# Kernel tuning notes

Measured on AMD Instinct MI355X. Metric: run time of the kernel, lower is better.

## Reference

```python
import jax, jax.numpy as jnp
import numpy as np

MULT = 0.001      # DEFAULT_MULTIPLIER
N_ITERS = 9       # self.N
N_K = 4           # self.l
BINARY = ('mul', 'add')  # original binary_ops_list order


def _valid_pairs(nc, r, lc):
    # replicate flag logic over (i, j) candidate pairs
    nri = N_ITERS - r
    out = []
    for i in range(nc - 1):
        for j in range(i + 1, nc):
            if nri == lc - 1:
                flag = i >= 3
            elif nri == lc:
                flag = j >= 3
            else:
                flag = nri > lc
            if flag:
                out.append((i, j))
    return out


def _act(name, res):
    if name == 'sigmoid':
        return MULT * jax.nn.sigmoid(res)
    if name == 'tanh':
        return MULT * jnp.tanh(res)
    if name == 'minus':
        return 1.0 - res
    return res  # identity


def run_cell(x, h_prev, L, R, b, w, plan=None):
    """Faithful RRNNforGRUCell tree-structure search.
    record mode (plan=None): data-dependent decisions taken concretely (eager).
    replay mode (plan given): purely differentiable jnp replay of recorded plan.
    """
    record = plan is None
    if record:
        plan = []
    xv = x.reshape(-1)
    hv = h_prev.reshape(-1)
    H = xv.shape[0]
    zero = jnp.zeros((H,), dtype=xv.dtype)
    G = []            # max_vector per iteration
    second = []       # second-ranked vector per iteration
    comp_src = []     # G-indices backing current components_list
    for r in range(N_ITERS):
        cand = [xv, hv, zero] + [G[g] for g in comp_src]
        nc = len(cand)
        C = jnp.stack(cand)                       # (nc, H)
        CL = jnp.einsum('ch,khd->ckd', C, L)      # (nc, 4, H) all s_i @ L_k
        CR = jnp.einsum('ch,khd->ckd', C, R)      # (nc, 4, H) all s_j @ R_k
        V = []
        if record:
            entries = []
            for (i, j) in _valid_pairs(nc, r, len(comp_src)):
                for k in range(N_K):
                    for bf in BINARY:
                        if bf == 'mul':
                            res = CL[i, k] * CR[j, k] + b[k]
                        else:
                            res = CL[i, k] + CR[j, k] + b[k]
                        if float(jnp.max(jnp.abs(res))) >= 1.0:
                            acts = ('sigmoid', 'tanh')
                        else:
                            acts = ('sigmoid', 'tanh', 'minus', 'identity')
                        for a in acts:
                            V.append(_act(a, res))
                            entries.append((i, j, k, bf, a))
        else:
            entries = plan[r]['entries']
            cache = {}
            for (i, j, k, bf, a) in entries:
                key = (i, j, k, bf)
                if key not in cache:
                    if bf == 'mul':
                        cache[key] = CL[i, k] * CR[j, k] + b[k]
                    else:
                        cache[key] = CL[i, k] + CR[j, k] + b[k]
                V.append(_act(a, cache[key]))
        Vs = jnp.stack(V)          # (nV, H)
        scores = Vs @ w            # (nV,) scoring Linear(H,1,bias=False)
        if record:
            s = np.asarray(scores)
            max_idx = int(np.argmax(s))
            # position of the element ranked second-smallest (original code)
            second_idx = int(np.where(np.argsort(s) == 1)[0][0])
            plan.append({'entries': entries, 'max_idx': max_idx, 'second_idx': second_idx})
        else:
            max_idx = plan[r]['max_idx']
            second_idx = plan[r]['second_idx']
        probs = jax.nn.softmax(scores)
        # NOTE: replicates original bug: loop uses stale `i` == nc-2, so every
        # v is weighted by probabilities[nc-2].
        max_vec = probs[nc - 2] * Vs.sum(axis=0)
        second.append(V[second_idx])
        G.append(max_vec)
        i, j = entries[max_idx][0], entries[max_idx][1]
        if i > 2 and j > 2:
            comp_src[i - 3] = r
            del comp_src[j - 3]
        elif i <= 2 and j > 2:
            comp_src[j - 3] = r
        else:
            comp_src.append(r)
    Gs = jnp.stack(G)                       # (9, H)
    out = (Gs[-1], Gs, Gs @ w, jnp.stack(second) @ w)
    return (out, plan) if record else out


def setup_inputs() -> dict:
    key = jax.random.key(0)
    ks = jax.random.split(key, 6)
    H = 2048
    return {
        'x': jax.random.normal(ks[0], (1, H), jnp.float32),
        'h_prev': jax.random.normal(ks[1], (1, H), jnp.float32),
        'L': MULT * jax.random.normal(ks[2], (N_K, H, H), jnp.float32),
        'R': MULT * jax.random.normal(ks[3], (N_K, H, H), jnp.float32),
        'b': MULT * jax.random.normal(ks[4], (N_K, H), jnp.float32),
        'w': jax.random.normal(ks[5], (H,), jnp.float32),
    }


def reference(x, h_prev, L, R, b, w):
    # returns (h_next, G_stack [9,H], scores of G [9], second_scores [9])
    out, _ = run_cell(x, h_prev, L, R, b, w)
    return out
```

## Files before the change

kernel.cpp:

```cpp
#include <hip/hip_runtime.h>
#include <math.h>

#define HDIM 2048
#define NK 4
#define NIT 9
#define NSID 11
#define MAXPAIRS 36
#define MAXBASES (MAXPAIRS*8)

#define CACHE_SZ (NSID*2*NK*HDIM)
#define OFF_CACHE 0
#define OFF_AMAX   (OFF_CACHE + CACHE_SZ)
#define OFF_DOTR_D (OFF_AMAX + MAXBASES)
#define OFF_DOTS_D (OFF_DOTR_D + 2*MAXBASES)
#define OFF_DOTT_D (OFF_DOTS_D + 2*MAXBASES)
#define PLAN_SZ 152
#define OFF_PLAN0 (OFF_DOTT_D + 2*MAXBASES)
#define OFF_PLAN1 (OFF_PLAN0 + PLAN_SZ)
#define OFF_SEL   (OFF_PLAN1 + PLAN_SZ)
#define OFF_STATE (OFF_SEL + 16)
#define OFF_SUMW_D (OFF_STATE + 16)
#define OFF_GT8   (OFF_SUMW_D + 16)
#define OFF_PART  (OFF_GT8 + 8*HDIM)

#define SEL_PSEL 0
#define SEL_C4   1

__device__ __forceinline__ float wredmax(float v){
#pragma unroll
  for(int o=32;o;o>>=1) v = fmaxf(v,__shfl_down(v,o,64));
  return v;
}
__device__ __forceinline__ float wredsum(float v){
#pragma unroll
  for(int o=32;o;o>>=1) v += __shfl_down(v,o,64);
  return v;
}
__device__ __forceinline__ double wredsumd(double v){
#pragma unroll
  for(int o=32;o;o>>=1) v += __shfl_down(v,o,64);
  return v;
}

__device__ void build_plan(int r, int lc, const int* cs, int* plan){
  int nc = 3 + lc;
  int nri = NIT - r;
  int np = 0;
  for(int i=0;i<nc-1;i++){
    for(int j=i+1;j<nc;j++){
      bool flag;
      if (nri == lc-1)      flag = (i>=3);
      else if (nri == lc)   flag = (j>=3);
      else                  flag = (nri > lc);
      if(flag){
        plan[8+np]            = i;
        plan[8+MAXPAIRS+np]   = j;
        plan[8+2*MAXPAIRS+np] = (i<3)? i : 3+cs[i-3];
        plan[8+3*MAXPAIRS+np] = (j<3)? j : 3+cs[j-3];
        np++;
      }
    }
  }
  plan[0]=nc; plan[1]=np; plan[2]=np*8;
}

__global__ __launch_bounds__(256) void kinit(const float* __restrict__ w,
                                             float* __restrict__ ws,
                                             float* __restrict__ out){
  for(int i=blockIdx.x*256+threadIdx.x; i<8*HDIM; i+=gridDim.x*256)
    ws[OFF_CACHE + 16*HDIM + i] = 0.f;
  if (blockIdx.x == 0){
    double s = 0.0;
    for(int d=threadIdx.x; d<HDIM; d+=256) s += (double)w[d];
    s = wredsumd(s);
    __shared__ double red[4];
    int wv = threadIdx.x>>6, ln = threadIdx.x&63;
    if(!ln) red[wv]=s;
    __syncthreads();
    if(threadIdx.x==0){
      *(double*)(ws + OFF_SUMW_D) = red[0]+red[1]+red[2]+red[3];
      int* st = (int*)(ws + OFF_STATE);
      for(int q=0;q<=8;q++) st[q]=0;
      build_plan(0, 0, st+1, (int*)(ws + OFF_PLAN0));
    }
    if (threadIdx.x < 18) out[10*HDIM + threadIdx.x] = 0.f;
  }
}

__global__ __launch_bounds__(256) void kvecmat(const float* __restrict__ v,
                                               const float* __restrict__ L,
                                               const float* __restrict__ R,
                                               float* __restrict__ ws){
  __shared__ float vs[64];
  int combo = blockIdx.x >> 6;
  int m = combo >> 2, k = combo & 3;
  int rem = blockIdx.x & 63;
  int hc = rem >> 1, dc = rem & 1;
  int h0 = hc*64;
  int d0 = dc*1024 + threadIdx.x*4;
  if (threadIdx.x < 64) vs[threadIdx.x] = v[h0 + threadIdx.x];
  __syncthreads();
  const float* M = (m==0?L:R) + (size_t)k*HDIM*HDIM;
  float ax=0.f, ay=0.f, az=0.f, aw=0.f;
#pragma unroll 8
  for(int h=0; h<64; h++){
    const float4 f = *reinterpret_cast<const float4*>(M + (size_t)(h0+h)*HDIM + d0);
    float vv = vs[h];
    ax = fmaf(vv, f.x, ax); ay = fmaf(vv, f.y, ay);
    az = fmaf(vv, f.z, az); aw = fmaf(vv, f.w, aw);
  }
  float4 o; o.x=ax; o.y=ay; o.z=az; o.w=aw;
  *reinterpret_cast<float4*>(ws + OFF_PART + ((size_t)combo*32 + hc)*HDIM + d0) = o;
}

__global__ __launch_bounds__(256) void kreduce(float* __restrict__ ws, int sid){
  int combo = blockIdx.x >> 3;
  int dc = blockIdx.x & 7;
  int d = dc*256 + threadIdx.x;
  const float* p = ws + OFF_PART + (size_t)combo*32*HDIM + d;
  float s = 0.f;
#pragma unroll
  for(int hc=0; hc<32; hc++) s += p[(size_t)hc*HDIM];
  int m = combo>>2, k = combo&3;
  ws[OFF_CACHE + ((size_t)(sid*2+m)*NK + k)*HDIM + d] = s;
}

__global__ __launch_bounds__(256) void kbasestats(const float* __restrict__ bvec,
                                                  const float* __restrict__ w,
                                                  float* __restrict__ ws, int par){
  const int* plan = (const int*)(ws + (par ? OFF_PLAN1 : OFF_PLAN0));
  int nb = plan[2];
  int t = blockIdx.x;
  if (t >= nb) return;
  int p = t>>3, k=(t>>1)&3, bf=t&1;
  int si = plan[8+2*MAXPAIRS+p], sj = plan[8+3*MAXPAIRS+p];
  const float* CL = ws + OFF_CACHE + ((size_t)(si*2+0)*NK + k)*HDIM;
  const float* CR = ws + OFF_CACHE + ((size_t)(sj*2+1)*NK + k)*HDIM;
  const float* bk = bvec + (size_t)k*HDIM;
  float am=0.f; double dr=0.0, ds=0.0, dt=0.0;
  for(int d=threadIdx.x; d<HDIM; d+=256){
    float a = CL[d], c = CR[d];
    float res = (bf==0) ? __fadd_rn(__fmul_rn(a,c), bk[d])
                        : __fadd_rn(__fadd_rn(a,c), bk[d]);
    float wd = w[d];
    am = fmaxf(am, fabsf(res));
    float sg = 1.0f/(1.0f+expf(-res));
    float th = tanhf(res);
    dr += (double)res*(double)wd;
    ds += (double)sg *(double)wd;
    dt += (double)th *(double)wd;
  }
  am = wredmax(am); dr = wredsumd(dr); ds = wredsumd(ds); dt = wredsumd(dt);
  __shared__ double redd[4][3];
  __shared__ float  redm[4];
  int wv = threadIdx.x>>6, ln = threadIdx.x&63;
  if(!ln){ redm[wv]=am; redd[wv][0]=dr; redd[wv][1]=ds; redd[wv][2]=dt; }
  __syncthreads();
  if(!threadIdx.x){
    float A=redm[0]; double Dr=redd[0][0], Ds=redd[0][1], Dt=redd[0][2];
    for(int q=1;q<4;q++){ A=fmaxf(A,redm[q]); Dr+=redd[q][0]; Ds+=redd[q][1]; Dt+=redd[q][2]; }
    ws[OFF_AMAX+t]=A;
    ((double*)(ws+OFF_DOTR_D))[t]=Dr;
    ((double*)(ws+OFF_DOTS_D))[t]=Ds;
    ((double*)(ws+OFF_DOTT_D))[t]=Dt;
  }
}

__global__ __launch_bounds__(256) void kselect(float* __restrict__ ws,
                                               float* __restrict__ out, int r){
  __shared__ double s4[MAXBASES][4];
  __shared__ int    sna[MAXBASES];
  __shared__ double tval[256];
  __shared__ int    tidx[256];
  __shared__ double tz[256];
  __shared__ int    tcnt[256];
  __shared__ double sh_smax;
  int par = r & 1;
  int* plan = (int*)(ws + (par ? OFF_PLAN1 : OFF_PLAN0));
  int nc = plan[0];
  int nb = plan[2];
  double sumw = *(const double*)(ws + OFF_SUMW_D);
  const double* DR = (const double*)(ws+OFF_DOTR_D);
  const double* DS = (const double*)(ws+OFF_DOTS_D);
  const double* DT = (const double*)(ws+OFF_DOTT_D);
  int tid = threadIdx.x;
  for(int t=tid; t<nb; t+=256){
    float A  = ws[OFF_AMAX+t];
    double Dr = DR[t], Ds = DS[t], Dt = DT[t];
    sna[t] = (A < 1.0f) ? 4 : 2;
    s4[t][0] = 0.001*Ds;
    s4[t][1] = 0.001*Dt;
    s4[t][2] = sumw - Dr;
    s4[t][3] = Dr;
  }
  __syncthreads();
  double best = -1e300; int bidx = 1<<30;
  for(int q=tid; q<nb*4; q+=256){
    int t=q>>2, a=q&3;
    if (a < sna[t]){
      double v = s4[t][a];
      if (v > best || (v==best && q < bidx)){ best=v; bidx=q; }
    }
  }
  tval[tid]=best; tidx[tid]=bidx;
  __syncthreads();
  if (tid==0){
    double bb=tval[0]; int bi=tidx[0];
    for(int u=1;u<256;u++)
      if (tval[u] > bb || (tval[u]==bb && tidx[u] < bi)){ bb=tval[u]; bi=tidx[u]; }
    sh_smax = bb;
    tidx[0] = bi;
  }
  __syncthreads();
  double smax = sh_smax;
  double s1 = s4[0][1];
  double z = 0.0; int cnt = 0;
  for(int q=tid; q<nb*4; q+=256){
    int t=q>>2, a=q&3;
    if (a < sna[t]){
      double v = s4[t][a];
      z += exp(v - smax);
      cnt += (v < s1) ? 1 : 0;
    }
  }
  tz[tid]=z; tcnt[tid]=cnt;
  __syncthreads();
  if (tid==0){
    int bi = tidx[0];
    double Z=0.0; int rank=0;
    for(int u=0;u<256;u++){ Z += tz[u]; rank += tcnt[u]; }
    int need = nc-2, e=0; double s_sel=0.0;
    for(int t=0;t<nb;t++){
      int n = sna[t];
      if (need < e+n){ s_sel = s4[t][need-e]; break; }
      e += n;
    }
    double psel = exp(s_sel - smax) / Z;
    int e2=0; double ssec=0.0;
    for(int t=0;t<nb;t++){
      int n = sna[t];
      if (rank < e2+n){ ssec = s4[t][rank-e2]; break; }
      e2 += n;
    }
    out[10*HDIM + 9 + r] = (float)ssec;
    int c4=0;
    for(int t=0;t<nb;t++) c4 += (sna[t]==4) ? 1 : 0;
    int mt = bi>>2;
    int mp = mt>>3;
    int ci = plan[8+mp], cj = plan[8+MAXPAIRS+mp];
    float* sel = ws + OFF_SEL;
    int*  seli = (int*)sel;
    sel[SEL_PSEL] = (float)psel;
    seli[SEL_C4]  = c4;
    int* st = (int*)(ws + OFF_STATE);
    int lc = st[0];
    int* cs = st+1;
    if (ci>2 && cj>2){
      cs[ci-3] = r;
      for(int q2=cj-3; q2<lc-1; q2++) cs[q2]=cs[q2+1];
      lc--;
    } else if (ci<=2 && cj>2){
      cs[cj-3] = r;
    } else {
      cs[lc] = r; lc++;
    }
    st[0]=lc;
    if (r+1 < NIT)
      build_plan(r+1, lc, cs, (int*)(ws + ((par^1) ? OFF_PLAN1 : OFF_PLAN0)));
  }
}

__global__ __launch_bounds__(256) void kaccum(const float* __restrict__ bvec,
                                              float* __restrict__ ws, int r){
  int par = r & 1;
  const int* plan = (const int*)(ws + (par ? OFF_PLAN1 : OFF_PLAN0));
  int nb = plan[2];
  int bc = blockIdx.x >> 3;
  int db = blockIdx.x & 7;
  int d = db*256 + threadIdx.x;
  float acc = 0.f;
  for(int t=bc; t<nb; t+=8){
    int p=t>>3, k=(t>>1)&3, bf=t&1;
    int si = plan[8+2*MAXPAIRS+p], sj = plan[8+3*MAXPAIRS+p];
    float a = ws[OFF_CACHE + ((size_t)(si*2+0)*NK+k)*HDIM + d];
    float c = ws[OFF_CACHE + ((size_t)(sj*2+1)*NK+k)*HDIM + d];
    float res = (bf==0) ? (a*c + bvec[(size_t)k*HDIM+d]) : (a + c + bvec[(size_t)k*HDIM+d]);
    float ex  = __expf(-res);
    float sig = 1.0f/(1.0f+ex);
    float ex2 = ex*ex;
    float th  = (1.0f-ex2)/(1.0f+ex2);
    acc += sig + th;
  }
  ws[OFF_GT8 + (size_t)bc*HDIM + d] = acc;
}

__global__ __launch_bounds__(256) void kfinal(const float* __restrict__ w,
                                              float* __restrict__ ws,
                                              float* __restrict__ out, int r){
  int d = blockIdx.x*256 + threadIdx.x;
  const float* sel = ws + OFF_SEL;
  const int*  seli = (const int*)sel;
  float psel = sel[SEL_PSEL];
  int  c4   = seli[SEL_C4];
  float s = 0.f;
#pragma unroll
  for(int bc=0; bc<8; bc++) s += ws[OFF_GT8 + (size_t)bc*HDIM + d];
  float g = psel * (0.001f*s + (float)c4);
  out[HDIM + (size_t)r*HDIM + d] = g;
  if (r == NIT-1) out[d] = g;
  float gw = wredsum(g*w[d]);
  __shared__ float red[4];
  int wv = threadIdx.x>>6, ln = threadIdx.x&63;
  if(!ln) red[wv]=gw;
  __syncthreads();
  if(!threadIdx.x)
    atomicAdd(&out[10*HDIM + r], red[0]+red[1]+red[2]+red[3]);
}

extern "C" void kernel_launch(void* const* d_in, const int* in_sizes, int n_in,
                              void* d_out, int out_size, void* d_ws, size_t ws_size,
                              hipStream_t stream){
  const float* x = (const float*)d_in[0];
  const float* h = (const float*)d_in[1];
  const float* L = (const float*)d_in[2];
  const float* R = (const float*)d_in[3];
  const float* b = (const float*)d_in[4];
  const float* w = (const float*)d_in[5];
  float* out = (float*)d_out;
  float* ws  = (float*)d_ws;

  kinit<<<32,256,0,stream>>>(w, ws, out);
  kvecmat<<<512,256,0,stream>>>(x, L, R, ws);
  kreduce<<<64,256,0,stream>>>(ws, 0);
  kvecmat<<<512,256,0,stream>>>(h, L, R, ws);
  kreduce<<<64,256,0,stream>>>(ws, 1);
  for(int r=0;r<NIT;r++){
    if (r > 0){
      kvecmat<<<512,256,0,stream>>>(out + HDIM + (size_t)(r-1)*HDIM, L, R, ws);
      kreduce<<<64,256,0,stream>>>(ws, 3+(r-1));
    }
    kbasestats<<<MAXBASES,256,0,stream>>>(b, w, ws, r&1);
    kselect<<<1,256,0,stream>>>(ws, out, r);
    kaccum<<<64,256,0,stream>>>(b, ws, r);
    kfinal<<<8,256,0,stream>>>(w, ws, out, r);
  }
}
```

Before: 601.7 us.

## Fuse per-iteration kernels and batch initial vector-matrix products

Folds the init work into the first vecmat launch, runs the x and h vector-matrix products in one launch, and merges basestats with accum and select with final. This cuts the launch count per iteration from six to four and removes the atomic and workspace round-trip for the selection scalars. The vecmat tiling is also changed from float4 to float2 loads over smaller column chunks, doubling block count. kselfin now does the final pass with a single block, which serializes 2048 elements of work onto one block.

```diff
diff --git a/kernel.cpp b/kernel.cpp
--- a/kernel.cpp
+++ b/kernel.cpp
@@ -17,14 +17,10 @@
 #define PLAN_SZ 152
 #define OFF_PLAN0 (OFF_DOTT_D + 2*MAXBASES)
 #define OFF_PLAN1 (OFF_PLAN0 + PLAN_SZ)
-#define OFF_SEL   (OFF_PLAN1 + PLAN_SZ)
-#define OFF_STATE (OFF_SEL + 16)
+#define OFF_STATE (OFF_PLAN1 + PLAN_SZ)
 #define OFF_SUMW_D (OFF_STATE + 16)
 #define OFF_GT8   (OFF_SUMW_D + 16)
 #define OFF_PART  (OFF_GT8 + 8*HDIM)
-
-#define SEL_PSEL 0
-#define SEL_C4   1
 
 __device__ __forceinline__ float wredmax(float v){
 #pragma unroll
@@ -64,109 +60,136 @@
   plan[0]=nc; plan[1]=np; plan[2]=np*8;
 }
 
-__global__ __launch_bounds__(256) void kinit(const float* __restrict__ w,
-                                             float* __restrict__ ws,
-                                             float* __restrict__ out){
-  for(int i=blockIdx.x*256+threadIdx.x; i<8*HDIM; i+=gridDim.x*256)
-    ws[OFF_CACHE + 16*HDIM + i] = 0.f;
-  if (blockIdx.x == 0){
-    double s = 0.0;
-    for(int d=threadIdx.x; d<HDIM; d+=256) s += (double)w[d];
-    s = wredsumd(s);
-    __shared__ double red[4];
-    int wv = threadIdx.x>>6, ln = threadIdx.x&63;
-    if(!ln) red[wv]=s;
-    __syncthreads();
-    if(threadIdx.x==0){
-      *(double*)(ws + OFF_SUMW_D) = red[0]+red[1]+red[2]+red[3];
-      int* st = (int*)(ws + OFF_STATE);
-      for(int q=0;q<=8;q++) st[q]=0;
-      build_plan(0, 0, st+1, (int*)(ws + OFF_PLAN0));
-    }
-    if (threadIdx.x < 18) out[10*HDIM + threadIdx.x] = 0.f;
-  }
-}
-
-__global__ __launch_bounds__(256) void kvecmat(const float* __restrict__ v,
+__global__ __launch_bounds__(256) void kvecmat(const float* __restrict__ va,
+                                               const float* __restrict__ vb,
+                                               const float* __restrict__ w,
                                                const float* __restrict__ L,
                                                const float* __restrict__ R,
-                                               float* __restrict__ ws){
+                                               float* __restrict__ ws,
+                                               int nvec){
+  int bid = blockIdx.x;
+  int tid = threadIdx.x;
+  if (bid >= (nvec<<10)){
+    int ib = bid - (nvec<<10);
+    for(int i = ib*256+tid; i < 8*HDIM; i += 32*256)
+      ws[OFF_CACHE + 16*HDIM + i] = 0.f;
+    if (ib == 0){
+      double s = 0.0;
+      for(int d=tid; d<HDIM; d+=256) s += (double)w[d];
+      s = wredsumd(s);
+      __shared__ double red[4];
+      int wv = tid>>6, ln = tid&63;
+      if(!ln) red[wv]=s;
+      __syncthreads();
+      if(tid==0){
+        *(double*)(ws + OFF_SUMW_D) = red[0]+red[1]+red[2]+red[3];
+        int* st = (int*)(ws + OFF_STATE);
+        for(int q=0;q<=8;q++) st[q]=0;
+        build_plan(0, 0, st+1, (int*)(ws + OFF_PLAN0));
+      }
+    }
+    return;
+  }
+  int vec = bid >> 10;
+  int b   = bid & 1023;
+  int combo = b >> 7;
+  int hc    = (b >> 2) & 31;
+  int dc    = b & 3;
+  const float* v = vec ? vb : va;
   __shared__ float vs[64];
-  int combo = blockIdx.x >> 6;
-  int m = combo >> 2, k = combo & 3;
-  int rem = blockIdx.x & 63;
-  int hc = rem >> 1, dc = rem & 1;
-  int h0 = hc*64;
-  int d0 = dc*1024 + threadIdx.x*4;
-  if (threadIdx.x < 64) vs[threadIdx.x] = v[h0 + threadIdx.x];
-  __syncthreads();
-  const float* M = (m==0?L:R) + (size_t)k*HDIM*HDIM;
-  float ax=0.f, ay=0.f, az=0.f, aw=0.f;
+  if (tid < 64) vs[tid] = v[hc*64 + tid];
+  __syncthreads();
+  int m = combo>>2, k = combo&3;
+  const float* M = (m==0?L:R) + (size_t)k*HDIM*HDIM + (size_t)hc*64*HDIM + dc*512 + tid*2;
+  float ax=0.f, ay=0.f;
 #pragma unroll 8
   for(int h=0; h<64; h++){
-    const float4 f = *reinterpret_cast<const float4*>(M + (size_t)(h0+h)*HDIM + d0);
+    const float2 f = *reinterpret_cast<const float2*>(M + (size_t)h*HDIM);
     float vv = vs[h];
     ax = fmaf(vv, f.x, ax); ay = fmaf(vv, f.y, ay);
-    az = fmaf(vv, f.z, az); aw = fmaf(vv, f.w, aw);
-  }
-  float4 o; o.x=ax; o.y=ay; o.z=az; o.w=aw;
-  *reinterpret_cast<float4*>(ws + OFF_PART + ((size_t)combo*32 + hc)*HDIM + d0) = o;
-}
-
-__global__ __launch_bounds__(256) void kreduce(float* __restrict__ ws, int sid){
-  int combo = blockIdx.x >> 3;
-  int dc = blockIdx.x & 7;
-  int d = dc*256 + threadIdx.x;
-  const float* p = ws + OFF_PART + (size_t)combo*32*HDIM + d;
+  }
+  float2 o; o.x=ax; o.y=ay;
+  *reinterpret_cast<float2*>(ws + OFF_PART + ((size_t)(vec*8+combo)*32 + hc)*HDIM + dc*512 + tid*2) = o;
+}
+
+__global__ __launch_bounds__(256) void kreduce(float* __restrict__ ws, int sid0){
+  int b = blockIdx.x;
+  int vec = b>>6, rem = b&63;
+  int combo = rem>>3, dc8 = rem&7;
+  int d = dc8*256 + threadIdx.x;
+  const float* p = ws + OFF_PART + (size_t)(vec*8+combo)*32*HDIM + d;
   float s = 0.f;
 #pragma unroll
   for(int hc=0; hc<32; hc++) s += p[(size_t)hc*HDIM];
   int m = combo>>2, k = combo&3;
+  int sid = sid0 + vec;
   ws[OFF_CACHE + ((size_t)(sid*2+m)*NK + k)*HDIM + d] = s;
 }
 
-__global__ __launch_bounds__(256) void kbasestats(const float* __restrict__ bvec,
+__global__ __launch_bounds__(256) void kbaseaccum(const float* __restrict__ bvec,
                                                   const float* __restrict__ w,
                                                   float* __restrict__ ws, int par){
   const int* plan = (const int*)(ws + (par ? OFF_PLAN1 : OFF_PLAN0));
   int nb = plan[2];
-  int t = blockIdx.x;
-  if (t >= nb) return;
-  int p = t>>3, k=(t>>1)&3, bf=t&1;
-  int si = plan[8+2*MAXPAIRS+p], sj = plan[8+3*MAXPAIRS+p];
-  const float* CL = ws + OFF_CACHE + ((size_t)(si*2+0)*NK + k)*HDIM;
-  const float* CR = ws + OFF_CACHE + ((size_t)(sj*2+1)*NK + k)*HDIM;
-  const float* bk = bvec + (size_t)k*HDIM;
-  float am=0.f; double dr=0.0, ds=0.0, dt=0.0;
-  for(int d=threadIdx.x; d<HDIM; d+=256){
-    float a = CL[d], c = CR[d];
-    float res = (bf==0) ? __fadd_rn(__fmul_rn(a,c), bk[d])
-                        : __fadd_rn(__fadd_rn(a,c), bk[d]);
-    float wd = w[d];
-    am = fmaxf(am, fabsf(res));
-    float sg = 1.0f/(1.0f+expf(-res));
-    float th = tanhf(res);
-    dr += (double)res*(double)wd;
-    ds += (double)sg *(double)wd;
-    dt += (double)th *(double)wd;
-  }
-  am = wredmax(am); dr = wredsumd(dr); ds = wredsumd(ds); dt = wredsumd(dt);
-  __shared__ double redd[4][3];
-  __shared__ float  redm[4];
-  int wv = threadIdx.x>>6, ln = threadIdx.x&63;
-  if(!ln){ redm[wv]=am; redd[wv][0]=dr; redd[wv][1]=ds; redd[wv][2]=dt; }
-  __syncthreads();
-  if(!threadIdx.x){
-    float A=redm[0]; double Dr=redd[0][0], Ds=redd[0][1], Dt=redd[0][2];
-    for(int q=1;q<4;q++){ A=fmaxf(A,redm[q]); Dr+=redd[q][0]; Ds+=redd[q][1]; Dt+=redd[q][2]; }
-    ws[OFF_AMAX+t]=A;
-    ((double*)(ws+OFF_DOTR_D))[t]=Dr;
-    ((double*)(ws+OFF_DOTS_D))[t]=Ds;
-    ((double*)(ws+OFF_DOTT_D))[t]=Dt;
-  }
-}
-
-__global__ __launch_bounds__(256) void kselect(float* __restrict__ ws,
+  if (blockIdx.x < MAXBASES){
+    int t = blockIdx.x;
+    if (t >= nb) return;
+    int p = t>>3, k=(t>>1)&3, bf=t&1;
+    int si = plan[8+2*MAXPAIRS+p], sj = plan[8+3*MAXPAIRS+p];
+    const float* CL = ws + OFF_CACHE + ((size_t)(si*2+0)*NK + k)*HDIM;
+    const float* CR = ws + OFF_CACHE + ((size_t)(sj*2+1)*NK + k)*HDIM;
+    const float* bk = bvec + (size_t)k*HDIM;
+    float am=0.f; double dr=0.0, ds=0.0, dt=0.0;
+    for(int d=threadIdx.x; d<HDIM; d+=256){
+      float a = CL[d], c = CR[d];
+      float res = (bf==0) ? __fadd_rn(__fmul_rn(a,c), bk[d])
+                          : __fadd_rn(__fadd_rn(a,c), bk[d]);
+      float wd = w[d];
+      am = fmaxf(am, fabsf(res));
+      float sg = 1.0f/(1.0f+expf(-res));
+      float th = tanhf(res);
+      dr += (double)res*(double)wd;
+      ds += (double)sg *(double)wd;
+      dt += (double)th *(double)wd;
+    }
+    am = wredmax(am); dr = wredsumd(dr); ds = wredsumd(ds); dt = wredsumd(dt);
+    __shared__ double redd[4][3];
+    __shared__ float  redm[4];
+    int wv = threadIdx.x>>6, ln = threadIdx.x&63;
+    if(!ln){ redm[wv]=am; redd[wv][0]=dr; redd[wv][1]=ds; redd[wv][2]=dt; }
+    __syncthreads();
+    if(!threadIdx.x){
+      float A=redm[0]; double Dr=redd[0][0], Ds=redd[0][1], Dt=redd[0][2];
+      for(int q=1;q<4;q++){ A=fmaxf(A,redm[q]); Dr+=redd[q][0]; Ds+=redd[q][1]; Dt+=redd[q][2]; }
+      ws[OFF_AMAX+t]=A;
+      ((double*)(ws+OFF_DOTR_D))[t]=Dr;
+      ((double*)(ws+OFF_DOTS_D))[t]=Ds;
+      ((double*)(ws+OFF_DOTT_D))[t]=Dt;
+    }
+  } else {
+    int bid2 = blockIdx.x - MAXBASES;
+    int bc = bid2 >> 3;
+    int db = bid2 & 7;
+    int d = db*256 + threadIdx.x;
+    float acc = 0.f;
+    for(int t=bc; t<nb; t+=8){
+      int p=t>>3, k=(t>>1)&3, bf=t&1;
+      int si = plan[8+2*MAXPAIRS+p], sj = plan[8+3*MAXPAIRS+p];
+      float a = ws[OFF_CACHE + ((size_t)(si*2+0)*NK+k)*HDIM + d];
+      float c = ws[OFF_CACHE + ((size_t)(sj*2+1)*NK+k)*HDIM + d];
+      float res = (bf==0) ? (a*c + bvec[(size_t)k*HDIM+d]) : (a + c + bvec[(size_t)k*HDIM+d]);
+      float ex  = __expf(-res);
+      float sig = 1.0f/(1.0f+ex);
+      float ex2 = ex*ex;
+      float th  = (1.0f-ex2)/(1.0f+ex2);
+      acc += sig + th;
+    }
+    ws[OFF_GT8 + (size_t)bc*HDIM + d] = acc;
+  }
+}
+
+__global__ __launch_bounds__(256) void kselfin(const float* __restrict__ w,
+                                               float* __restrict__ ws,
                                                float* __restrict__ out, int r){
   __shared__ double s4[MAXBASES][4];
   __shared__ int    sna[MAXBASES];
@@ -175,6 +198,8 @@
   __shared__ double tz[256];
   __shared__ int    tcnt[256];
   __shared__ double sh_smax;
+  __shared__ float  sh_psel;
+  __shared__ int    sh_c4;
   int par = r & 1;
   int* plan = (int*)(ws + (par ? OFF_PLAN1 : OFF_PLAN0));
   int nc = plan[0];
@@ -248,10 +273,8 @@
     int mt = bi>>2;
     int mp = mt>>3;
     int ci = plan[8+mp], cj = plan[8+MAXPAIRS+mp];
-    float* sel = ws + OFF_SEL;
-    int*  seli = (int*)sel;
-    sel[SEL_PSEL] = (float)psel;
-    seli[SEL_C4]  = c4;
+    sh_psel = (float)psel;
+    sh_c4   = c4;
     int* st = (int*)(ws + OFF_STATE);
     int lc = st[0];
     int* cs = st+1;
@@ -268,53 +291,27 @@
     if (r+1 < NIT)
       build_plan(r+1, lc, cs, (int*)(ws + ((par^1) ? OFF_PLAN1 : OFF_PLAN0)));
   }
-}
-
-__global__ __launch_bounds__(256) void kaccum(const float* __restrict__ bvec,
-                                              float* __restrict__ ws, int r){
-  int par = r & 1;
-  const int* plan = (const int*)(ws + (par ? OFF_PLAN1 : OFF_PLAN0));
-  int nb = plan[2];
-  int bc = blockIdx.x >> 3;
-  int db = blockIdx.x & 7;
-  int d = db*256 + threadIdx.x;
-  float acc = 0.f;
-  for(int t=bc; t<nb; t+=8){
-    int p=t>>3, k=(t>>1)&3, bf=t&1;
-    int si = plan[8+2*MAXPAIRS+p], sj = plan[8+3*MAXPAIRS+p];
-    float a = ws[OFF_CACHE + ((size_t)(si*2+0)*NK+k)*HDIM + d];
-    float c = ws[OFF_CACHE + ((size_t)(sj*2+1)*NK+k)*HDIM + d];
-    float res = (bf==0) ? (a*c + bvec[(size_t)k*HDIM+d]) : (a + c + bvec[(size_t)k*HDIM+d]);
-    float ex  = __expf(-res);
-    float sig = 1.0f/(1.0f+ex);
-    float ex2 = ex*ex;
-    float th  = (1.0f-ex2)/(1.0f+ex2);
-    acc += sig + th;
-  }
-  ws[OFF_GT8 + (size_t)bc*HDIM + d] = acc;
-}
-
-__global__ __launch_bounds__(256) void kfinal(const float* __restrict__ w,
-                                              float* __restrict__ ws,
-                                              float* __restrict__ out, int r){
-  int d = blockIdx.x*256 + threadIdx.x;
-  const float* sel = ws + OFF_SEL;
-  const int*  seli = (const int*)sel;
-  float psel = sel[SEL_PSEL];
-  int  c4   = seli[SEL_C4];
-  float s = 0.f;
-#pragma unroll
-  for(int bc=0; bc<8; bc++) s += ws[OFF_GT8 + (size_t)bc*HDIM + d];
-  float g = psel * (0.001f*s + (float)c4);
-  out[HDIM + (size_t)r*HDIM + d] = g;
-  if (r == NIT-1) out[d] = g;
-  float gw = wredsum(g*w[d]);
-  __shared__ float red[4];
-  int wv = threadIdx.x>>6, ln = threadIdx.x&63;
-  if(!ln) red[wv]=gw;
-  __syncthreads();
-  if(!threadIdx.x)
-    atomicAdd(&out[10*HDIM + r], red[0]+red[1]+red[2]+red[3]);
+  __syncthreads();
+  float psel = sh_psel;
+  float c4f  = (float)sh_c4;
+  float dot = 0.f;
+#pragma unroll
+  for(int q=0;q<8;q++){
+    int d = q*256 + tid;
+    float s = 0.f;
+#pragma unroll
+    for(int bc=0; bc<8; bc++) s += ws[OFF_GT8 + (size_t)bc*HDIM + d];
+    float g = psel * (0.001f*s + c4f);
+    out[HDIM + (size_t)r*HDIM + d] = g;
+    if (r == NIT-1) out[d] = g;
+    dot = fmaf(g, w[d], dot);
+  }
+  dot = wredsum(dot);
+  __shared__ float redf[4];
+  int wv = tid>>6, ln = tid&63;
+  if(!ln) redf[wv]=dot;
+  __syncthreads();
+  if(!tid) out[10*HDIM + r] = redf[0]+redf[1]+redf[2]+redf[3];
 }
 
 extern "C" void kernel_launch(void* const* d_in, const int* in_sizes, int n_in,
@@ -329,19 +326,14 @@
   float* out = (float*)d_out;
   float* ws  = (float*)d_ws;
 
-  kinit<<<32,256,0,stream>>>(w, ws, out);
-  kvecmat<<<512,256,0,stream>>>(x, L, R, ws);
-  kreduce<<<64,256,0,stream>>>(ws, 0);
-  kvecmat<<<512,256,0,stream>>>(h, L, R, ws);
-  kreduce<<<64,256,0,stream>>>(ws, 1);
+  kvecmat<<<2048+32,256,0,stream>>>(x, h, w, L, R, ws, 2);
+  kreduce<<<128,256,0,stream>>>(ws, 0);
   for(int r=0;r<NIT;r++){
     if (r > 0){
-      kvecmat<<<512,256,0,stream>>>(out + HDIM + (size_t)(r-1)*HDIM, L, R, ws);
+      kvecmat<<<1024,256,0,stream>>>(out + HDIM + (size_t)(r-1)*HDIM, nullptr, w, L, R, ws, 1);
       kreduce<<<64,256,0,stream>>>(ws, 3+(r-1));
     }
-    kbasestats<<<MAXBASES,256,0,stream>>>(b, w, ws, r&1);
-    kselect<<<1,256,0,stream>>>(ws, out, r);
-    kaccum<<<64,256,0,stream>>>(b, ws, r);
-    kfinal<<<8,256,0,stream>>>(w, ws, out, r);
-  }
-}
+    kbaseaccum<<<MAXBASES+64,256,0,stream>>>(b, w, ws, r&1);
+    kselfin<<<1,256,0,stream>>>(w, ws, out, r);
+  }
+}
```

New measurement: 582.7 us. 1.03x faster.
